# Optimization experiments

Measured on AMD Instinct MI355X. Metric: run time of the kernel, lower is better.

Reference implementation:

```python
import jax, jax.numpy as jnp
import numpy as np

DY = jnp.array([-1, -1, -1, 0, 0, 0, 1, 1, 1], dtype=jnp.float32)
DX = jnp.array([-1, 0, 1, -1, 0, 1, -1, 0, 1], dtype=jnp.float32)
REG = jnp.stack([DY, DX])  # (2,9) regular_matrix: row0 = dy, row1 = dx
EPS = 1e-5


def conv3x3(x, w, b):
    y = jax.lax.conv_general_dilated(x, w, (1, 1), ((1, 1), (1, 1)),
                                     dimension_numbers=('NCHW', 'OIHW', 'NCHW'))
    return y + b[None, :, None, None]


def batchnorm(x, gamma, beta):
    m = x.mean((0, 2, 3), keepdims=True)
    v = x.var((0, 2, 3), keepdims=True)
    return gamma[None, :, None, None] * (x - m) * jax.lax.rsqrt(v + EPS) + beta[None, :, None, None]


def make_offset(tm, tr):
    # tm: (N,4,H,W) per-pixel 2x2 matrix, tr: (N,2,H,W) translation
    N, _, H, W = tm.shape
    M = tm.transpose(0, 2, 3, 1).reshape(N, H, W, 2, 2)
    off = jnp.einsum('nhwij,jk->nhwik', M, REG) - REG          # (N,H,W,2,9)
    off = off.transpose(0, 4, 3, 1, 2)                          # (N,9,2,H,W)
    off = off + tr[:, None, :, :, :]                            # broadcast translation over K
    return off


def deform_conv(x, off, w):
    # x: (N,C,H,W), off: (N,9,2,H,W) with [...,0]=dy,[...,1]=dx, w: (Co,C,3,3)
    N, C, H, W = x.shape
    K = 9
    py = jnp.arange(H, dtype=x.dtype)[None, None, :, None] + DY[None, :, None, None] + off[:, :, 0]
    px = jnp.arange(W, dtype=x.dtype)[None, None, None, :] + DX[None, :, None, None] + off[:, :, 1]
    y0 = jnp.floor(py)
    x0 = jnp.floor(px)
    wy = py - y0
    wx = px - x0
    y0i = y0.astype(jnp.int32)
    x0i = x0.astype(jnp.int32)
    x_flat = x.reshape(N, C, H * W)

    def corner(yi, xi, wgt):
        valid = (yi >= 0) & (yi < H) & (xi >= 0) & (xi < W)
        idx = jnp.clip(yi, 0, H - 1) * W + jnp.clip(xi, 0, W - 1)   # (N,K,H,W)
        g = jax.vmap(lambda xf, ix: xf[:, ix])(x_flat, idx.reshape(N, -1))
        g = g.reshape(N, C, K, H, W)
        return g * (wgt * valid)[:, None]

    cols = (corner(y0i, x0i, (1 - wy) * (1 - wx))
            + corner(y0i, x0i + 1, (1 - wy) * wx)
            + corner(y0i + 1, x0i, wy * (1 - wx))
            + corner(y0i + 1, x0i + 1, wy * wx))
    Co = w.shape[0]
    return jnp.einsum('nckhw,ock->nohw', cols, w.reshape(Co, C, K))


def setup_inputs() -> dict:
    key = jax.random.key(0)
    ks = jax.random.split(key, 16)
    N, C, Co, H, W = 4, 256, 256, 64, 64
    s_off = 0.02   # small init so offsets stay near the regular grid
    s_w = 0.05
    return {
        'x': jax.random.normal(ks[0], (N, C, H, W), jnp.float32),
        'tm1_w': jax.random.normal(ks[1], (4, C, 3, 3), jnp.float32) * s_off,
        'tm1_b': jax.random.normal(ks[2], (4,), jnp.float32) * s_off,
        'tr1_w': jax.random.normal(ks[3], (2, C, 3, 3), jnp.float32) * s_off,
        'tr1_b': jax.random.normal(ks[4], (2,), jnp.float32) * s_off,
        'dcn1_w': jax.random.normal(ks[5], (Co, C, 3, 3), jnp.float32) * s_w,
        'bn1_g': jnp.ones((Co,), jnp.float32),
        'bn1_b': jnp.zeros((Co,), jnp.float32),
        'tm2_w': jax.random.normal(ks[6], (4, Co, 3, 3), jnp.float32) * s_off,
        'tm2_b': jax.random.normal(ks[7], (4,), jnp.float32) * s_off,
        'tr2_w': jax.random.normal(ks[8], (2, Co, 3, 3), jnp.float32) * s_off,
        'tr2_b': jax.random.normal(ks[9], (2,), jnp.float32) * s_off,
        'dcn2_w': jax.random.normal(ks[10], (Co, Co, 3, 3), jnp.float32) * s_w,
        'bn2_g': jnp.ones((Co,), jnp.float32),
        'bn2_b': jnp.zeros((Co,), jnp.float32),
    }


def reference(x, tm1_w, tm1_b, tr1_w, tr1_b, dcn1_w, bn1_g, bn1_b,
              tm2_w, tm2_b, tr2_w, tr2_b, dcn2_w, bn2_g, bn2_b):
    residual = x
    off1 = make_offset(conv3x3(x, tm1_w, tm1_b), conv3x3(x, tr1_w, tr1_b))
    out = deform_conv(x, off1, dcn1_w)
    out = jax.nn.relu(batchnorm(out, bn1_g, bn1_b))
    off2 = make_offset(conv3x3(out, tm2_w, tm2_b), conv3x3(out, tr2_w, tr2_b))
    out = deform_conv(out, off2, dcn2_w)
    out = batchnorm(out, bn2_g, bn2_b)
    return jax.nn.relu(out + residual)
```

## Files before the change

kernel.cpp:

```cpp
#include <hip/hip_runtime.h>
#include <hip/hip_bf16.h>

#define HH 64
#define WW 64
#define HWSZ 4096
#define NBATCH 4
#define CCH 256
#define NPIX 16384
#define CK 2304
#define EPSB 1e-5f

typedef __attribute__((ext_vector_type(8))) short bf16x8;
typedef __attribute__((ext_vector_type(4))) float f32x4;

static __device__ __forceinline__ unsigned short f2bf(float f){
  __hip_bfloat16 h = __float2bfloat16(f);
  return *(unsigned short*)&h;
}

#if __has_builtin(__builtin_amdgcn_global_load_lds)
#define GLD(S,D) __builtin_amdgcn_global_load_lds((const __attribute__((address_space(1))) void*)(S), \
                                                  (__attribute__((address_space(3))) void*)(D), 16, 0, 0)
#else
#define GLD(S,D) (*(bf16x8*)((char*)(D) + (threadIdx.x & 63)*16) = *(const bf16x8*)(S))
#endif

__global__ __launch_bounds__(256) void k_transpose_in(const float* __restrict__ x,
                                                      float* __restrict__ xT){
  __shared__ float tile[64][65];
  int hw0 = blockIdx.x * 64;
  int c0  = blockIdx.y * 64;
  int n   = blockIdx.z;
  int t = threadIdx.x;
  int col = t & 63, rb = t >> 6;
#pragma unroll
  for (int r = 0; r < 16; ++r){
    int cl = rb + r*4;
    tile[cl][col] = x[(size_t)(n*CCH + c0 + cl)*HWSZ + hw0 + col];
  }
  __syncthreads();
#pragma unroll
  for (int r = 0; r < 16; ++r){
    int hwl = rb + r*4;
    xT[(size_t)(n*HWSZ + hw0 + hwl)*CCH + c0 + col] = tile[col][hwl];
  }
}

__global__ void k_woff_perm(const float* __restrict__ tmw, const float* __restrict__ trw,
                            float* __restrict__ woff){
  int idx = blockIdx.x*256 + threadIdx.x;
  if (idx >= 9*6*CCH) return;
  int k = idx / (6*CCH); int rem = idx % (6*CCH); int j = rem >> 8; int c = rem & 255;
  float v = (j < 4) ? tmw[(size_t)(j*CCH + c)*9 + k]
                    : trw[(size_t)((j-4)*CCH + c)*9 + k];
  woff[idx] = v;
}

__global__ void k_wgemm_perm(const float* __restrict__ w, __hip_bfloat16* __restrict__ wp){
  int idx = blockIdx.x*256 + threadIdx.x;
  if (idx >= CCH*CK) return;
  int blk = idx >> 13;
  int e   = idx & 8191;
  int o   = e >> 5;
  int el  = e & 31;
  int tap = blk >> 3, cb = blk & 7;
  int c   = cb*32 + (el ^ (((o >> 1) & 3) << 3));
  wp[idx] = __float2bfloat16(w[(size_t)o*CK + c*9 + tap]);
}

__global__ __launch_bounds__(256) void k_offsets(const float* __restrict__ src,
    const float* __restrict__ wofft, const float* __restrict__ tmb,
    const float* __restrict__ trb, float* __restrict__ off){
  int t = threadIdx.x;
  int wid = t >> 6, lane = t & 63;
  int pbase = blockIdx.x*32 + wid*8;
  int n = pbase >> 12; int hw = pbase & 4095; int h = hw >> 6; int w0 = hw & 63;
  const float* base = src + (size_t)n*HWSZ*CCH + lane*4;

  float acc[8][6];
#pragma unroll
  for (int pi = 0; pi < 8; ++pi)
#pragma unroll
    for (int j = 0; j < 6; ++j) acc[pi][j] = 0.f;

  for (int k = 0; k < 9; ++k){
    int ky = k/3 - 1, kx = k%3 - 1;
    int yy = h + ky;
    if (yy < 0 || yy >= HH) continue;
    float4 wv[6];
#pragma unroll
    for (int j = 0; j < 6; ++j)
      wv[j] = *(const float4*)(wofft + ((k*6 + j) << 8) + lane*4);
#pragma unroll
    for (int pi = 0; pi < 8; ++pi){
      int xx = w0 + pi + kx;
      if (xx < 0 || xx >= WW) continue;
      float4 s4 = *(const float4*)(base + (size_t)(yy*WW + xx)*CCH);
#pragma unroll
      for (int j = 0; j < 6; ++j)
        acc[pi][j] += s4.x*wv[j].x + s4.y*wv[j].y + s4.z*wv[j].z + s4.w*wv[j].w;
    }
  }

#pragma unroll
  for (int pi = 0; pi < 8; ++pi)
#pragma unroll
    for (int j = 0; j < 6; ++j){
      float v = acc[pi][j];
#pragma unroll
      for (int m = 32; m >= 1; m >>= 1) v += __shfl_xor(v, m);
      acc[pi][j] = v;
    }

  float b0 = tmb[0], b1 = tmb[1], b2 = tmb[2], b3 = tmb[3];
  float c0 = trb[0], c1 = trb[1];
  if (lane < 18){
    int k = lane >> 1, comp = lane & 1;
    float dy = (float)(k/3 - 1), dx = (float)(k%3 - 1);
#pragma unroll
    for (int pi = 0; pi < 8; ++pi){
      int p = pbase + pi;
      float val;
      if (comp == 0)
        val = (acc[pi][0] + b0)*dy + (acc[pi][1] + b1)*dx - dy + acc[pi][4] + c0;
      else
        val = (acc[pi][2] + b2)*dy + (acc[pi][3] + b3)*dx - dx + acc[pi][5] + c1;
      off[((size_t)p*9 + k)*2 + comp] = val;
    }
  }
}

struct Gset { float4 a, b, c, d; };

__global__ __launch_bounds__(256) void k_dcn(const float* __restrict__ src,
    const float* __restrict__ off, const __hip_bfloat16* __restrict__ wp,
    float* __restrict__ gout, float* __restrict__ pbstats){
  __shared__ __hip_bfloat16 Al[2*32*32];
  __shared__ __hip_bfloat16 Bl[2*256*32];
  __shared__ __align__(16) int   t_off[288][4];
  __shared__ __align__(16) float t_w[288][4];

  int t = threadIdx.x;
  int bid = blockIdx.x;
  int tile = (bid & 7)*64 + (bid >> 3);
  int pbase = tile * 32;

  for (int s = t; s < 288; s += 256){
    int px = s / 9, k = s - px*9;
    int p = pbase + px;
    int n = p >> 12; int hw = p & 4095; int h = hw >> 6; int w = hw & 63;
    float2 of = *(const float2*)(off + ((size_t)p*9 + k)*2);
    float py = (float)(h + k/3 - 1) + of.x;
    float px_ = (float)(w + (k - (k/3)*3) - 1) + of.y;
    float y0f = floorf(py), x0f = floorf(px_);
    float wy = py - y0f, wx = px_ - x0f;
    int y0 = (int)y0f, x0 = (int)x0f;
    int y1 = y0 + 1, x1 = x0 + 1;
    float w00 = (1.f-wy)*(1.f-wx), w01 = (1.f-wy)*wx;
    float w10 = wy*(1.f-wx),       w11 = wy*wx;
    if (y0 < 0 || y0 >= HH) { w00 = 0.f; w01 = 0.f; }
    if (y1 < 0 || y1 >= HH) { w10 = 0.f; w11 = 0.f; }
    if (x0 < 0 || x0 >= WW) { w00 = 0.f; w10 = 0.f; }
    if (x1 < 0 || x1 >= WW) { w01 = 0.f; w11 = 0.f; }
    int y0c = min(max(y0,0),HH-1), y1c = min(max(y1,0),HH-1);
    int x0c = min(max(x0,0),WW-1), x1c = min(max(x1,0),WW-1);
    int pbix = n << 12;
    t_off[s][0] = (pbix + y0c*WW + x0c) << 10;
    t_off[s][1] = (pbix + y0c*WW + x1c) << 10;
    t_off[s][2] = (pbix + y1c*WW + x0c) << 10;
    t_off[s][3] = (pbix + y1c*WW + x1c) << 10;
    t_w[s][0] = w00; t_w[s][1] = w01; t_w[s][2] = w10; t_w[s][3] = w11;
  }
  __syncthreads();

  int wid = t >> 6, lane = t & 63;
  int pxl = t >> 3, q = t & 7;
  const char* sbase = (const char*)src;
  const char* wpb = (const char*)wp;

  int abyte = pxl*64 + (((q >> 1) ^ ((pxl >> 1) & 3)) << 4) + (q & 1)*8;

  int kq = lane >> 4, fr = lane & 15;
  int abr0, abr1, bbr0, bbr1, bbr2, bbr3;
  {
    int a0 = 0*16 + fr;  abr0 = a0*64 + ((kq ^ ((a0 >> 1) & 3)) << 4);
    int a1 = 1*16 + fr;  abr1 = a1*64 + ((kq ^ ((a1 >> 1) & 3)) << 4);
    int o0 = wid*64 + 0*16 + fr;  bbr0 = o0*64 + ((kq ^ ((o0 >> 1) & 3)) << 4);
    int o1 = wid*64 + 1*16 + fr;  bbr1 = o1*64 + ((kq ^ ((o1 >> 1) & 3)) << 4);
    int o2 = wid*64 + 2*16 + fr;  bbr2 = o2*64 + ((kq ^ ((o2 >> 1) & 3)) << 4);
    int o3 = wid*64 + 3*16 + fr;  bbr3 = o3*64 + ((kq ^ ((o3 >> 1) & 3)) << 4);
  }

  f32x4 acc[2][4];
#pragma unroll
  for (int i = 0; i < 2; ++i)
#pragma unroll
    for (int j = 0; j < 4; ++j)
      acc[i][j] = (f32x4){0.f,0.f,0.f,0.f};

  Gset gA, gB;

  auto issue_gather = [&](int ktn, Gset& g){
    int slot = pxl*9 + (ktn >> 3);
    int chb = ((ktn & 7) << 7) + (q << 4);
    int4 o4 = *(const int4*)t_off[slot];
    g.a = *(const float4*)(sbase + (size_t)(unsigned)(o4.x + chb));
    g.b = *(const float4*)(sbase + (size_t)(unsigned)(o4.y + chb));
    g.c = *(const float4*)(sbase + (size_t)(unsigned)(o4.z + chb));
    g.d = *(const float4*)(sbase + (size_t)(unsigned)(o4.w + chb));
  };
  auto convert_write = [&](int ktc, Gset& g){
    int slot = pxl*9 + (ktc >> 3);
    float4 wv = *(const float4*)t_w[slot];
    float v0 = wv.x*g.a.x + wv.y*g.b.x + wv.z*g.c.x + wv.w*g.d.x;
    float v1 = wv.x*g.a.y + wv.y*g.b.y + wv.z*g.c.y + wv.w*g.d.y;
    float v2 = wv.x*g.a.z + wv.y*g.b.z + wv.z*g.c.z + wv.w*g.d.z;
    float v3 = wv.x*g.a.w + wv.y*g.b.w + wv.z*g.c.w + wv.w*g.d.w;
    ushort4 st; st.x = f2bf(v0); st.y = f2bf(v1); st.z = f2bf(v2); st.w = f2bf(v3);
    *(ushort4*)((char*)Al + (ktc & 1)*2048 + abyte) = st;
  };
  auto issue_B = [&](int ktb){
    const char* bsrc = wpb + (size_t)ktb*16384 + t*16;
    char* bdst = (char*)Bl + (ktb & 1)*16384 + wid*1024;
    GLD(bsrc,                bdst);
    GLD(bsrc + 4096,         bdst + 4096);
    GLD(bsrc + 8192,         bdst + 8192);
    GLD(bsrc + 12288,        bdst + 12288);
  };

  issue_B(0);
  asm volatile("" ::: "memory");
  issue_gather(0, gA);
  issue_gather(1, gB);
  convert_write(0, gA);
  __syncthreads();

  auto body = [&](int kt, Gset& gIss, Gset& gCnv){
    const char* Ac = (const char*)Al + (kt & 1)*2048;
    const char* Bc = (const char*)Bl + (kt & 1)*16384;
    bf16x8 av0 = *(const bf16x8*)(Ac + abr0);
    bf16x8 av1 = *(const bf16x8*)(Ac + abr1);
    bf16x8 bv0 = *(const bf16x8*)(Bc + bbr0);
    bf16x8 bv1 = *(const bf16x8*)(Bc + bbr1);
    bf16x8 bv2 = *(const bf16x8*)(Bc + bbr2);
    bf16x8 bv3 = *(const bf16x8*)(Bc + bbr3);
    if (kt <= 70) issue_B(kt + 1);
    asm volatile("" ::: "memory");
    if (kt <= 69) issue_gather(kt + 2, gIss);
    acc[0][0] = __builtin_amdgcn_mfma_f32_16x16x32_bf16(av0, bv0, acc[0][0], 0, 0, 0);
    acc[0][1] = __builtin_amdgcn_mfma_f32_16x16x32_bf16(av0, bv1, acc[0][1], 0, 0, 0);
    acc[0][2] = __builtin_amdgcn_mfma_f32_16x16x32_bf16(av0, bv2, acc[0][2], 0, 0, 0);
    acc[0][3] = __builtin_amdgcn_mfma_f32_16x16x32_bf16(av0, bv3, acc[0][3], 0, 0, 0);
    acc[1][0] = __builtin_amdgcn_mfma_f32_16x16x32_bf16(av1, bv0, acc[1][0], 0, 0, 0);
    acc[1][1] = __builtin_amdgcn_mfma_f32_16x16x32_bf16(av1, bv1, acc[1][1], 0, 0, 0);
    acc[1][2] = __builtin_amdgcn_mfma_f32_16x16x32_bf16(av1, bv2, acc[1][2], 0, 0, 0);
    acc[1][3] = __builtin_amdgcn_mfma_f32_16x16x32_bf16(av1, bv3, acc[1][3], 0, 0, 0);
    if (kt <= 70) convert_write(kt + 1, gCnv);
    __syncthreads();
  };

  for (int kk = 0; kk < 72; kk += 2){
    body(kk + 0, gA, gB);
    body(kk + 1, gB, gA);
  }

#pragma unroll
  for (int mi = 0; mi < 2; ++mi)
#pragma unroll
    for (int ni = 0; ni < 4; ++ni){
      int rr = pbase + mi*16 + kq*4;
      int cc = wid*64 + ni*16 + fr;
#pragma unroll
      for (int r = 0; r < 4; ++r)
        gout[(size_t)(rr + r)*CCH + cc] = acc[mi][ni][r];
    }
#pragma unroll
  for (int ni = 0; ni < 4; ++ni){
    float s = 0.f, ss = 0.f;
#pragma unroll
    for (int mi = 0; mi < 2; ++mi)
#pragma unroll
      for (int r = 0; r < 4; ++r){
        float v = acc[mi][ni][r];
        s += v; ss += v*v;
      }
    s  += __shfl_xor(s, 16);  s  += __shfl_xor(s, 32);
    ss += __shfl_xor(ss, 16); ss += __shfl_xor(ss, 32);
    if (kq == 0){
      int cc = wid*64 + ni*16 + fr;
      pbstats[(size_t)cc*512 + bid]         = s;
      pbstats[(size_t)(256 + cc)*512 + bid] = ss;
    }
  }
}

__global__ __launch_bounds__(256) void k_stats_reduce(const float* __restrict__ pb,
                                                      float* __restrict__ so){
  __shared__ float red[32][8];
  int t = threadIdx.x;
  int g = t >> 3, j = t & 7;
  int o = blockIdx.x*32 + g;
  const float4* p = (const float4*)(pb + (size_t)o*512 + j*64);
  float s = 0.f;
#pragma unroll
  for (int i = 0; i < 16; ++i){
    float4 v = p[i];
    s += v.x + v.y + v.z + v.w;
  }
  red[g][j] = s;
  __syncthreads();
  if (j == 0){
    float a = 0.f;
#pragma unroll
    for (int i = 0; i < 8; ++i) a += red[g][i];
    so[o] = a;
  }
}

__global__ __launch_bounds__(256) void k_bn_apply(const float* __restrict__ v,
    const float* __restrict__ stats, const float* __restrict__ g,
    const float* __restrict__ bb, float* __restrict__ y){
  const float inv = 1.f/16384.f;
  for (size_t i = (size_t)blockIdx.x*256 + threadIdx.x; i < (size_t)NPIX*CCH;
       i += (size_t)gridDim.x*256){
    int c = (int)(i & 255);
    float mean = stats[c]*inv;
    float var  = stats[CCH + c]*inv - mean*mean;
    float sc = g[c]*rsqrtf(var + EPSB);
    float sh = bb[c] - mean*sc;
    float val = fmaf(v[i], sc, sh);
    y[i] = val > 0.f ? val : 0.f;
  }
}

__global__ __launch_bounds__(256) void k_final(const float* __restrict__ v,
    const float* __restrict__ stats, const float* __restrict__ g,
    const float* __restrict__ bb, const float* __restrict__ x,
    float* __restrict__ out){
  __shared__ float tile[64][65];
  int hw0 = blockIdx.x * 64;
  int o0  = blockIdx.y * 64;
  int n   = blockIdx.z;
  int t = threadIdx.x;
  int col = t & 63, rb = t >> 6;
  const float inv = 1.f/16384.f;
#pragma unroll
  for (int r = 0; r < 16; ++r){
    int pl = rb + r*4;
    tile[pl][col] = v[(size_t)(n*HWSZ + hw0 + pl)*CCH + o0 + col];
  }
  __syncthreads();
#pragma unroll
  for (int r = 0; r < 16; ++r){
    int ol = rb + r*4;
    int o = o0 + ol;
    float mean = stats[o]*inv;
    float var  = stats[CCH + o]*inv - mean*mean;
    float sc = g[o]*rsqrtf(var + EPSB);
    float sh = bb[o] - mean*sc;
    size_t gi = (size_t)(n*CCH + o)*HWSZ + hw0 + col;
    float val = fmaf(tile[col][ol], sc, sh) + x[gi];
    out[gi] = val > 0.f ? val : 0.f;
  }
}

extern "C" void kernel_launch(void* const* d_in, const int* in_sizes, int n_in,
                              void* d_out, int out_size, void* d_ws, size_t ws_size,
                              hipStream_t stream){
  const float* x     = (const float*)d_in[0];
  const float* tm1_w = (const float*)d_in[1];
  const float* tm1_b = (const float*)d_in[2];
  const float* tr1_w = (const float*)d_in[3];
  const float* tr1_b = (const float*)d_in[4];
  const float* dcn1_w= (const float*)d_in[5];
  const float* bn1_g = (const float*)d_in[6];
  const float* bn1_b = (const float*)d_in[7];
  const float* tm2_w = (const float*)d_in[8];
  const float* tm2_b = (const float*)d_in[9];
  const float* tr2_w = (const float*)d_in[10];
  const float* tr2_b = (const float*)d_in[11];
  const float* dcn2_w= (const float*)d_in[12];
  const float* bn2_g = (const float*)d_in[13];
  const float* bn2_b = (const float*)d_in[14];
  float* out = (float*)d_out;

  char* ws = (char*)d_ws;
  size_t cursor = 0;
  auto alloc = [&](size_t bytes)->char*{
    char* p = ws + cursor; cursor += (bytes + 255) & ~(size_t)255; return p;
  };
  float* xT    = (float*)alloc((size_t)NPIX*CCH*4);
  float* ybuf  = (float*)alloc((size_t)NPIX*CCH*4);
  float* gout  = (float*)alloc((size_t)NPIX*CCH*4);
  float* offb  = (float*)alloc((size_t)NPIX*9*2*4);
  float* woff1 = (float*)alloc(9*6*CCH*4);
  float* woff2 = (float*)alloc(9*6*CCH*4);
  __hip_bfloat16* wg1 = (__hip_bfloat16*)alloc((size_t)CCH*CK*2);
  __hip_bfloat16* wg2 = (__hip_bfloat16*)alloc((size_t)CCH*CK*2);
  float* stats = (float*)alloc(1024*4);
  float* pbstats = (float*)alloc((size_t)512*512*4);

  k_transpose_in<<<dim3(64,4,4),256,0,stream>>>(x, xT);
  k_woff_perm<<<54,256,0,stream>>>(tm1_w, tr1_w, woff1);
  k_woff_perm<<<54,256,0,stream>>>(tm2_w, tr2_w, woff2);
  k_wgemm_perm<<<2304,256,0,stream>>>(dcn1_w, wg1);
  k_wgemm_perm<<<2304,256,0,stream>>>(dcn2_w, wg2);

  k_offsets<<<512,256,0,stream>>>(xT, woff1, tm1_b, tr1_b, offb);
  k_dcn<<<512,256,0,stream>>>(xT, offb, wg1, gout, pbstats);
  k_stats_reduce<<<16,256,0,stream>>>(pbstats, stats);
  k_bn_apply<<<2048,256,0,stream>>>(gout, stats, bn1_g, bn1_b, ybuf);

  k_offsets<<<512,256,0,stream>>>(ybuf, woff2, tm2_b, tr2_b, offb);
  k_dcn<<<512,256,0,stream>>>(ybuf, offb, wg2, gout, pbstats);
  k_stats_reduce<<<16,256,0,stream>>>(pbstats, stats + 512);
  k_final<<<dim3(64,4,4),256,0,stream>>>(gout, stats + 512, bn2_g, bn2_b, x, out);
}
```

Before: 193.5 us.

## Store transposed activations in fp16 to halve gather and offset-conv traffic

The channel-last copies of the input and of the first BN output are now stored as fp16 instead of fp32. The offset convolution and the deformable gather read half as many bytes and convert to float in registers. The BN-apply kernel is also vectorised to process four channels per thread and write fp16. This cuts memory and L2 traffic in the gather-heavy kernels, at the cost of fp16 rounding of activations before the offset computation, which could perturb sampling positions.

Result: slower. 198.2 us (+2.4%).

```diff
diff --git a/kernel.cpp b/kernel.cpp
--- a/kernel.cpp
+++ b/kernel.cpp
@@ -1,5 +1,6 @@
 #include <hip/hip_runtime.h>
 #include <hip/hip_bf16.h>
+#include <hip/hip_fp16.h>
 
 #define HH 64
 #define WW 64
@@ -17,6 +18,14 @@
   __hip_bfloat16 h = __float2bfloat16(f);
   return *(unsigned short*)&h;
 }
+static __device__ __forceinline__ float hfu(unsigned short u){
+  __half h = *(__half*)&u;
+  return __half2float(h);
+}
+static __device__ __forceinline__ unsigned short f2h(float f){
+  __half h = __float2half(f);
+  return *(unsigned short*)&h;
+}
 
 #if __has_builtin(__builtin_amdgcn_global_load_lds)
 #define GLD(S,D) __builtin_amdgcn_global_load_lds((const __attribute__((address_space(1))) void*)(S), \
@@ -26,7 +35,7 @@
 #endif
 
 __global__ __launch_bounds__(256) void k_transpose_in(const float* __restrict__ x,
-                                                      float* __restrict__ xT){
+                                                      __half* __restrict__ xTh){
   __shared__ float tile[64][65];
   int hw0 = blockIdx.x * 64;
   int c0  = blockIdx.y * 64;
@@ -42,7 +51,7 @@
 #pragma unroll
   for (int r = 0; r < 16; ++r){
     int hwl = rb + r*4;
-    xT[(size_t)(n*HWSZ + hw0 + hwl)*CCH + c0 + col] = tile[col][hwl];
+    xTh[(size_t)(n*HWSZ + hw0 + hwl)*CCH + c0 + col] = __float2half(tile[col][hwl]);
   }
 }
 
@@ -68,14 +77,14 @@
   wp[idx] = __float2bfloat16(w[(size_t)o*CK + c*9 + tap]);
 }
 
-__global__ __launch_bounds__(256) void k_offsets(const float* __restrict__ src,
+__global__ __launch_bounds__(256) void k_offsets(const __half* __restrict__ src,
     const float* __restrict__ wofft, const float* __restrict__ tmb,
     const float* __restrict__ trb, float* __restrict__ off){
   int t = threadIdx.x;
   int wid = t >> 6, lane = t & 63;
   int pbase = blockIdx.x*32 + wid*8;
   int n = pbase >> 12; int hw = pbase & 4095; int h = hw >> 6; int w0 = hw & 63;
-  const float* base = src + (size_t)n*HWSZ*CCH + lane*4;
+  const __half* base = src + (size_t)n*HWSZ*CCH + lane*4;
 
   float acc[8][6];
 #pragma unroll
@@ -95,10 +104,11 @@
     for (int pi = 0; pi < 8; ++pi){
       int xx = w0 + pi + kx;
       if (xx < 0 || xx >= WW) continue;
-      float4 s4 = *(const float4*)(base + (size_t)(yy*WW + xx)*CCH);
+      ushort4 s4 = *(const ushort4*)(base + (size_t)(yy*WW + xx)*CCH);
+      float f0 = hfu(s4.x), f1 = hfu(s4.y), f2 = hfu(s4.z), f3 = hfu(s4.w);
 #pragma unroll
       for (int j = 0; j < 6; ++j)
-        acc[pi][j] += s4.x*wv[j].x + s4.y*wv[j].y + s4.z*wv[j].z + s4.w*wv[j].w;
+        acc[pi][j] += f0*wv[j].x + f1*wv[j].y + f2*wv[j].z + f3*wv[j].w;
     }
   }
 
@@ -130,9 +140,9 @@
   }
 }
 
-struct Gset { float4 a, b, c, d; };
-
-__global__ __launch_bounds__(256) void k_dcn(const float* __restrict__ src,
+struct Gset { ushort4 a, b, c, d; };
+
+__global__ __launch_bounds__(256) void k_dcn(const __half* __restrict__ src,
     const float* __restrict__ off, const __hip_bfloat16* __restrict__ wp,
     float* __restrict__ gout, float* __restrict__ pbstats){
   __shared__ __hip_bfloat16 Al[2*32*32];
@@ -165,10 +175,10 @@
     int y0c = min(max(y0,0),HH-1), y1c = min(max(y1,0),HH-1);
     int x0c = min(max(x0,0),WW-1), x1c = min(max(x1,0),WW-1);
     int pbix = n << 12;
-    t_off[s][0] = (pbix + y0c*WW + x0c) << 10;
-    t_off[s][1] = (pbix + y0c*WW + x1c) << 10;
-    t_off[s][2] = (pbix + y1c*WW + x0c) << 10;
-    t_off[s][3] = (pbix + y1c*WW + x1c) << 10;
+    t_off[s][0] = (pbix + y0c*WW + x0c) << 9;
+    t_off[s][1] = (pbix + y0c*WW + x1c) << 9;
+    t_off[s][2] = (pbix + y1c*WW + x0c) << 9;
+    t_off[s][3] = (pbix + y1c*WW + x1c) << 9;
     t_w[s][0] = w00; t_w[s][1] = w01; t_w[s][2] = w10; t_w[s][3] = w11;
   }
   __syncthreads();
@@ -202,20 +212,20 @@
 
   auto issue_gather = [&](int ktn, Gset& g){
     int slot = pxl*9 + (ktn >> 3);
-    int chb = ((ktn & 7) << 7) + (q << 4);
+    int chb = ((ktn & 7) << 6) + (q << 3);
     int4 o4 = *(const int4*)t_off[slot];
-    g.a = *(const float4*)(sbase + (size_t)(unsigned)(o4.x + chb));
-    g.b = *(const float4*)(sbase + (size_t)(unsigned)(o4.y + chb));
-    g.c = *(const float4*)(sbase + (size_t)(unsigned)(o4.z + chb));
-    g.d = *(const float4*)(sbase + (size_t)(unsigned)(o4.w + chb));
+    g.a = *(const ushort4*)(sbase + (size_t)(unsigned)(o4.x + chb));
+    g.b = *(const ushort4*)(sbase + (size_t)(unsigned)(o4.y + chb));
+    g.c = *(const ushort4*)(sbase + (size_t)(unsigned)(o4.z + chb));
+    g.d = *(const ushort4*)(sbase + (size_t)(unsigned)(o4.w + chb));
   };
   auto convert_write = [&](int ktc, Gset& g){
     int slot = pxl*9 + (ktc >> 3);
     float4 wv = *(const float4*)t_w[slot];
-    float v0 = wv.x*g.a.x + wv.y*g.b.x + wv.z*g.c.x + wv.w*g.d.x;
-    float v1 = wv.x*g.a.y + wv.y*g.b.y + wv.z*g.c.y + wv.w*g.d.y;
-    float v2 = wv.x*g.a.z + wv.y*g.b.z + wv.z*g.c.z + wv.w*g.d.z;
-    float v3 = wv.x*g.a.w + wv.y*g.b.w + wv.z*g.c.w + wv.w*g.d.w;
+    float v0 = wv.x*hfu(g.a.x) + wv.y*hfu(g.b.x) + wv.z*hfu(g.c.x) + wv.w*hfu(g.d.x);
+    float v1 = wv.x*hfu(g.a.y) + wv.y*hfu(g.b.y) + wv.z*hfu(g.c.y) + wv.w*hfu(g.d.y);
+    float v2 = wv.x*hfu(g.a.z) + wv.y*hfu(g.b.z) + wv.z*hfu(g.c.z) + wv.w*hfu(g.d.z);
+    float v3 = wv.x*hfu(g.a.w) + wv.y*hfu(g.b.w) + wv.z*hfu(g.c.w) + wv.w*hfu(g.d.w);
     ushort4 st; st.x = f2bf(v0); st.y = f2bf(v1); st.z = f2bf(v2); st.w = f2bf(v3);
     *(ushort4*)((char*)Al + (ktc & 1)*2048 + abyte) = st;
   };
@@ -319,17 +329,27 @@
 
 __global__ __launch_bounds__(256) void k_bn_apply(const float* __restrict__ v,
     const float* __restrict__ stats, const float* __restrict__ g,
-    const float* __restrict__ bb, float* __restrict__ y){
+    const float* __restrict__ bb, __half* __restrict__ y){
   const float inv = 1.f/16384.f;
-  for (size_t i = (size_t)blockIdx.x*256 + threadIdx.x; i < (size_t)NPIX*CCH;
-       i += (size_t)gridDim.x*256){
-    int c = (int)(i & 255);
-    float mean = stats[c]*inv;
-    float var  = stats[CCH + c]*inv - mean*mean;
-    float sc = g[c]*rsqrtf(var + EPSB);
-    float sh = bb[c] - mean*sc;
-    float val = fmaf(v[i], sc, sh);
-    y[i] = val > 0.f ? val : 0.f;
+  const size_t total = (size_t)NPIX*CCH/4;
+  for (size_t i4 = (size_t)blockIdx.x*256 + threadIdx.x; i4 < total;
+       i4 += (size_t)gridDim.x*256){
+    float4 vv = *(const float4*)&v[i4*4];
+    int c = (int)((i4 & 63) << 2);
+    float r[4] = {vv.x, vv.y, vv.z, vv.w};
+    ushort4 st;
+    unsigned short o[4];
+#pragma unroll
+    for (int j = 0; j < 4; ++j){
+      float mean = stats[c+j]*inv;
+      float var  = stats[CCH + c+j]*inv - mean*mean;
+      float sc = g[c+j]*rsqrtf(var + EPSB);
+      float sh = bb[c+j] - mean*sc;
+      float val = fmaf(r[j], sc, sh);
+      o[j] = f2h(val > 0.f ? val : 0.f);
+    }
+    st.x = o[0]; st.y = o[1]; st.z = o[2]; st.w = o[3];
+    *(ushort4*)&y[i4*4] = st;
   }
 }
 
@@ -389,8 +409,8 @@
   auto alloc = [&](size_t bytes)->char*{
     char* p = ws + cursor; cursor += (bytes + 255) & ~(size_t)255; return p;
   };
-  float* xT    = (float*)alloc((size_t)NPIX*CCH*4);
-  float* ybuf  = (float*)alloc((size_t)NPIX*CCH*4);
+  __half* xTh = (__half*)alloc((size_t)NPIX*CCH*2);
+  __half* ybh = (__half*)alloc((size_t)NPIX*CCH*2);
   float* gout  = (float*)alloc((size_t)NPIX*CCH*4);
   float* offb  = (float*)alloc((size_t)NPIX*9*2*4);
   float* woff1 = (float*)alloc(9*6*CCH*4);
@@ -400,19 +420,19 @@
   float* stats = (float*)alloc(1024*4);
   float* pbstats = (float*)alloc((size_t)512*512*4);
 
-  k_transpose_in<<<dim3(64,4,4),256,0,stream>>>(x, xT);
+  k_transpose_in<<<dim3(64,4,4),256,0,stream>>>(x, xTh);
   k_woff_perm<<<54,256,0,stream>>>(tm1_w, tr1_w, woff1);
   k_woff_perm<<<54,256,0,stream>>>(tm2_w, tr2_w, woff2);
   k_wgemm_perm<<<2304,256,0,stream>>>(dcn1_w, wg1);
   k_wgemm_perm<<<2304,256,0,stream>>>(dcn2_w, wg2);
 
-  k_offsets<<<512,256,0,stream>>>(xT, woff1, tm1_b, tr1_b, offb);
-  k_dcn<<<512,256,0,stream>>>(xT, offb, wg1, gout, pbstats);
+  k_offsets<<<512,256,0,stream>>>(xTh, woff1, tm1_b, tr1_b, offb);
+  k_dcn<<<512,256,0,stream>>>(xTh, offb, wg1, gout, pbstats);
   k_stats_reduce<<<16,256,0,stream>>>(pbstats, stats);
-  k_bn_apply<<<2048,256,0,stream>>>(gout, stats, bn1_g, bn1_b, ybuf);
-
-  k_offsets<<<512,256,0,stream>>>(ybuf, woff2, tm2_b, tr2_b, offb);
-  k_dcn<<<512,256,0,stream>>>(ybuf, offb, wg2, gout, pbstats);
+  k_bn_apply<<<2048,256,0,stream>>>(gout, stats, bn1_g, bn1_b, ybh);
+
+  k_offsets<<<512,256,0,stream>>>(ybh, woff2, tm2_b, tr2_b, offb);
+  k_dcn<<<512,256,0,stream>>>(ybh, offb, wg2, gout, pbstats);
   k_stats_reduce<<<16,256,0,stream>>>(pbstats, stats + 512);
   k_final<<<dim3(64,4,4),256,0,stream>>>(gout, stats + 512, bn2_g, bn2_b, x, out);
 }
```
